# Kernel optimization log

Measured on AMD Instinct MI355X. Metric: run time of the kernel, lower is better.

Reference implementation:

```python
import jax, jax.numpy as jnp
import numpy as np

EPS = 1e-8
TAU = 0.2
IOU_THR = 0.5
NEG = -1e9
N, C, H, D_FG, D_CLS = 8192, 1024, 256, 64, 128


def setup_inputs() -> dict:
    key = jax.random.key(0)
    ks = jax.random.split(key, 11)
    def lin(k, fan_in, fan_out):
        return jax.random.normal(k, (fan_in, fan_out), jnp.float32) / np.sqrt(fan_in)
    return {
        "roi_feats": jax.random.normal(ks[0], (N, C), jnp.float32),
        "labels": jax.random.randint(ks[1], (N,), 0, 21, jnp.int32).astype(jnp.int64),
        "ious": jax.random.uniform(ks[2], (N,), jnp.float32),
        "fg_w1": lin(ks[3], C, H), "fg_b1": jnp.zeros((H,), jnp.float32),
        "fg_w2": lin(ks[4], H, D_FG), "fg_b2": jnp.zeros((D_FG,), jnp.float32),
        "cls_w1": lin(ks[5], C, H), "cls_b1": jnp.zeros((H,), jnp.float32),
        "cls_w2": lin(ks[6], H, D_CLS), "cls_b2": jnp.zeros((D_CLS,), jnp.float32),
    }


def _project_normalize(x, w1, b1, w2, b2):
    h = jax.nn.relu(x @ w1 + b1)
    z = h @ w2 + b2
    norm = jnp.maximum(jnp.linalg.norm(z, axis=1, keepdims=True), EPS)
    return z / norm


def _forward(roi_feats, labels, ious, fg_w1, fg_b1, fg_w2, fg_b2, cls_w1, cls_b1, cls_w2, cls_b2):
    n = roi_feats.shape[0]
    z_fg = _project_normalize(roi_feats, fg_w1, fg_b1, fg_w2, fg_b2)
    z_cls = _project_normalize(roi_feats, cls_w1, cls_b1, cls_w2, cls_b2)

    ignore = labels == -1
    fg = (labels > 0) & ~ignore
    iou_weight = jnp.where(ious > IOU_THR, ious, 0.0)
    eye = jnp.eye(n, dtype=bool)

    # ---- fg/bg contrastive (bg_as_negatives_only=True) ----
    sim_fg = (z_fg @ z_fg.T) / TAU                       # [N,N]
    exp_sim = jnp.exp(sim_fg)
    denom = jnp.sum(exp_sim * (~eye).astype(jnp.float32), axis=1)
    pos = (fg & ~ignore)[None, :] & ~eye                 # positives: fg columns, no self
    n_pos = jnp.sum(pos, axis=1)
    numer = jnp.sum(exp_sim * pos.astype(jnp.float32), axis=1)
    # original computes den = denom + EPS then -log((numer+EPS)/(den+EPS))
    loss_i = -jnp.log((numer + EPS) / (denom + 2.0 * EPS))
    valid = (fg & ~ignore) & (n_pos > 0)
    w = iou_weight * valid.astype(jnp.float32)
    loss_fg_bg = jnp.sum(w * loss_i) / (jnp.sum(w) + EPS)

    # ---- class supervised contrastive ----
    sim_cls = (z_cls @ z_cls.T) / TAU
    sim_masked = jnp.where(eye, NEG, sim_cls)
    log_denom = jax.nn.logsumexp(sim_masked, axis=1)     # [N]
    log_p = jnp.where(eye, NEG, sim_cls - log_denom[:, None])
    # pos_mask keeps diagonal (as in original): same label, col not ignore, col label != 0
    posc = (labels[None, :] == labels[:, None]) & (~ignore)[None, :] & (labels[None, :] != 0)
    n_posc = jnp.sum(posc, axis=1).astype(jnp.float32)
    sum_log_p = jnp.sum(log_p * posc.astype(jnp.float32), axis=1)
    valid_c = (fg & ~ignore) & (n_posc > 0) & jnp.isfinite(log_denom)
    Lzi = jnp.where(valid_c, -sum_log_p / (n_posc + EPS), 0.0)
    wc = iou_weight * valid_c.astype(jnp.float32)
    loss_supcon = jnp.sum(wc * Lzi) / (jnp.sum(wc) + EPS)

    return jnp.stack([loss_fg_bg, loss_supcon])


def reference(roi_feats, labels, ious, fg_w1, fg_b1, fg_w2, fg_b2, cls_w1, cls_b1, cls_w2, cls_b2):
    return _forward(roi_feats, labels, ious, fg_w1, fg_b1, fg_w2, fg_b2, cls_w1, cls_b1, cls_w2, cls_b2)
```

## Files before the change

### kernel.cpp

```cpp
#include <hip/hip_runtime.h>


typedef __attribute__((ext_vector_type(8))) short bs8;
typedef __attribute__((ext_vector_type(4))) float f4;

#define MFMA_BF16(a, b, c) __builtin_amdgcn_mfma_f32_16x16x32_bf16((a), (b), (c), 0, 0, 0)

#if defined(__has_builtin)
#if __has_builtin(__builtin_amdgcn_exp2f)
#define EXP2F(x) __builtin_amdgcn_exp2f(x)
#endif
#endif
#ifndef EXP2F
#define EXP2F(x) exp2f(x)
#endif

#define K_LOG2E 7.2134752044448170f

__device__ __forceinline__ unsigned short f2bf(float f) {
  unsigned int u = __float_as_uint(f);
  u = (u + 0x7fffu + ((u >> 16) & 1u)) >> 16;
  return (unsigned short)u;
}
__device__ __forceinline__ float bf2f(unsigned short s) {
  return __uint_as_float(((unsigned int)s) << 16);
}

constexpr size_t O_W1T  = 0;
constexpr size_t O_W2TF = 1048576;
constexpr size_t O_W2TC = 1081344;
constexpr size_t O_H    = 1146880;
constexpr size_t O_ZF   = 9535488;
constexpr size_t O_ZC   = 10584064;
constexpr size_t O_SCLS = 12681216;
constexpr size_t O_ROWD = 12697600;
constexpr size_t O_ROWN = 12730368;
constexpr size_t O_ROWS = 12763136;
constexpr size_t O_SCAL = 12795904;
constexpr size_t O_HIST = 12795920;
constexpr size_t O_NFG  = 12796048;
constexpr int ZERO_WORDS = (int)((O_NFG + 4 - O_SCLS) / 4);

__global__ void __launch_bounds__(256) zero_kernel(float* __restrict__ p, int n) {
  int i = blockIdx.x * 256 + threadIdx.x;
  if (i < n) p[i] = 0.f;
}

__global__ void __launch_bounds__(256) transp_kernel(
    const float* __restrict__ fgw1, const float* __restrict__ clsw1,
    const float* __restrict__ fgw2, const float* __restrict__ clsw2,
    unsigned short* __restrict__ W1T, unsigned short* __restrict__ W2Tf,
    unsigned short* __restrict__ W2Tc) {
  __shared__ float tile[64][65];
  const int m = blockIdx.y;
  const float* src;
  unsigned short* dst;
  int R, C;
  if (m == 0)      { src = fgw1;  dst = W1T;              R = 1024; C = 256; }
  else if (m == 1) { src = clsw1; dst = W1T + 256 * 1024; R = 1024; C = 256; }
  else if (m == 2) { src = fgw2;  dst = W2Tf;             R = 256;  C = 64;  }
  else             { src = clsw2; dst = W2Tc;             R = 256;  C = 128; }
  const int cT = C >> 6;
  if (blockIdx.x >= (R >> 6) * cT) return;
  const int r0 = (blockIdx.x / cT) << 6, c0 = (blockIdx.x % cT) << 6;
  const int t = threadIdx.x;
  {
    const int rr = t >> 4, cc = (t & 15) << 2;
#pragma unroll
    for (int i = 0; i < 4; i++) {
      float4 v = *(const float4*)(src + (size_t)(r0 + rr + i * 16) * C + c0 + cc);
      tile[rr + i * 16][cc] = v.x; tile[rr + i * 16][cc + 1] = v.y;
      tile[rr + i * 16][cc + 2] = v.z; tile[rr + i * 16][cc + 3] = v.w;
    }
  }
  __syncthreads();
  {
    const int dr = t >> 2, dc = (t & 3) << 4;
    bs8 o0, o1;
#pragma unroll
    for (int j = 0; j < 8; j++) o0[j] = (short)f2bf(tile[dc + j][dr]);
#pragma unroll
    for (int j = 0; j < 8; j++) o1[j] = (short)f2bf(tile[dc + 8 + j][dr]);
    unsigned short* dp = dst + (size_t)(c0 + dr) * R + r0 + dc;
    *(bs8*)dp = o0;
    *(bs8*)(dp + 8) = o1;
  }
}

__global__ void __launch_bounds__(256) meta_kernel(const int* __restrict__ labels,
                                                   int* __restrict__ hist,
                                                   int* __restrict__ nfg) {
  __shared__ int sh[33];
  const int t = threadIdx.x;
  if (t < 33) sh[t] = 0;
  __syncthreads();
  int lab = labels[blockIdx.x * 256 + t];
  if (lab >= 0 && lab < 32) atomicAdd(&sh[lab], 1);
  if (lab > 0) atomicAdd(&sh[32], 1);
  __syncthreads();
  if (t < 32 && sh[t] > 0) atomicAdd(&hist[t], sh[t]);
  if (t == 32 && sh[32] > 0) atomicAdd(nfg, sh[32]);
}

__global__ void __launch_bounds__(256) gemm1_kernel(
    const float* __restrict__ X, const unsigned short* __restrict__ W1T,
    const float* __restrict__ b1f, const float* __restrict__ b1c,
    unsigned short* __restrict__ H) {
  __shared__ __align__(16) unsigned short lA[64 * 40];
  __shared__ __align__(16) unsigned short lB[128 * 40];
  const int t = threadIdx.x;
  const int w = t >> 6, lane = t & 63, ln = lane & 15, quad = lane >> 4;
  const int m0 = blockIdx.x * 64, n0 = blockIdx.y * 128;

  f4 acc[8];
#pragma unroll
  for (int s = 0; s < 8; s++) acc[s] = (f4){0.f, 0.f, 0.f, 0.f};

  for (int k0 = 0; k0 < 1024; k0 += 32) {
    __syncthreads();
    {
      const int r = t >> 2, c = (t & 3) * 8;
      const float* xp = X + (size_t)(m0 + r) * 1024 + k0 + c;
      float4 x0 = *(const float4*)xp;
      float4 x1 = *(const float4*)(xp + 4);
      bs8 av;
      av[0] = (short)f2bf(x0.x); av[1] = (short)f2bf(x0.y);
      av[2] = (short)f2bf(x0.z); av[3] = (short)f2bf(x0.w);
      av[4] = (short)f2bf(x1.x); av[5] = (short)f2bf(x1.y);
      av[6] = (short)f2bf(x1.z); av[7] = (short)f2bf(x1.w);
      *(bs8*)&lA[r * 40 + c] = av;
    }
#pragma unroll
    for (int i = 0; i < 2; i++) {
      const int ch = t + i * 256;
      const int r = ch >> 2, c = (ch & 3) * 8;
      *(bs8*)&lB[r * 40 + c] = *(const bs8*)(W1T + (size_t)(n0 + r) * 1024 + k0 + c);
    }
    __syncthreads();
    bs8 af = *(const bs8*)&lA[(w * 16 + ln) * 40 + quad * 8];
#pragma unroll
    for (int s = 0; s < 8; s++) {
      bs8 bf = *(const bs8*)&lB[(s * 16 + ln) * 40 + quad * 8];
      acc[s] = MFMA_BF16(af, bf, acc[s]);
    }
  }
#pragma unroll
  for (int s = 0; s < 8; s++) {
    const int n = n0 + s * 16 + ln;
    const float b = (n < 256) ? b1f[n] : b1c[n - 256];
#pragma unroll
    for (int r = 0; r < 4; r++) {
      float v = fmaxf(acc[s][r] + b, 0.f);
      H[(size_t)(m0 + w * 16 + quad * 4 + r) * 512 + n] = f2bf(v);
    }
  }
}

__global__ void __launch_bounds__(256) gemm2_kernel(
    const unsigned short* __restrict__ H,
    const unsigned short* __restrict__ W2Tf, const unsigned short* __restrict__ W2Tc,
    const float* __restrict__ b2f, const float* __restrict__ b2c,
    unsigned short* __restrict__ Zf, unsigned short* __restrict__ Zc) {
  const int t = threadIdx.x;
  const int w = t >> 6, lane = t & 63, ln = lane & 15, quad = lane >> 4;
  const int rw = blockIdx.x * 32 + (w & 1) * 16;

  if (w < 2) {
    const unsigned short* hrow = H + (size_t)(rw + ln) * 512;
    f4 acc[4];
#pragma unroll
    for (int s = 0; s < 4; s++) acc[s] = (f4){0.f, 0.f, 0.f, 0.f};
#pragma unroll
    for (int ks = 0; ks < 8; ks++) {
      bs8 af = *(const bs8*)(hrow + ks * 32 + quad * 8);
#pragma unroll
      for (int s = 0; s < 4; s++) {
        bs8 bf = *(const bs8*)(W2Tf + (size_t)(s * 16 + ln) * 256 + ks * 32 + quad * 8);
        acc[s] = MFMA_BF16(af, bf, acc[s]);
      }
    }
    float ss[4] = {0.f, 0.f, 0.f, 0.f};
#pragma unroll
    for (int s = 0; s < 4; s++) {
      float b = b2f[s * 16 + ln];
#pragma unroll
      for (int r = 0; r < 4; r++) {
        acc[s][r] += b;
        ss[r] = fmaf(acc[s][r], acc[s][r], ss[r]);
      }
    }
#pragma unroll
    for (int r = 0; r < 4; r++) {
#pragma unroll
      for (int off = 1; off < 16; off <<= 1) ss[r] += __shfl_xor(ss[r], off, 64);
      float sc = 1.f / fmaxf(sqrtf(ss[r]), 1e-8f);
#pragma unroll
      for (int s = 0; s < 4; s++)
        Zf[(size_t)(rw + quad * 4 + r) * 64 + s * 16 + ln] = f2bf(acc[s][r] * sc);
    }
  } else {
    const unsigned short* hrow = H + (size_t)(rw + ln) * 512 + 256;
    f4 acc[8];
#pragma unroll
    for (int s = 0; s < 8; s++) acc[s] = (f4){0.f, 0.f, 0.f, 0.f};
#pragma unroll
    for (int ks = 0; ks < 8; ks++) {
      bs8 af = *(const bs8*)(hrow + ks * 32 + quad * 8);
#pragma unroll
      for (int s = 0; s < 8; s++) {
        bs8 bf = *(const bs8*)(W2Tc + (size_t)(s * 16 + ln) * 256 + ks * 32 + quad * 8);
        acc[s] = MFMA_BF16(af, bf, acc[s]);
      }
    }
    float ss[4] = {0.f, 0.f, 0.f, 0.f};
#pragma unroll
    for (int s = 0; s < 8; s++) {
      float b = b2c[s * 16 + ln];
#pragma unroll
      for (int r = 0; r < 4; r++) {
        acc[s][r] += b;
        ss[r] = fmaf(acc[s][r], acc[s][r], ss[r]);
      }
    }
#pragma unroll
    for (int r = 0; r < 4; r++) {
#pragma unroll
      for (int off = 1; off < 16; off <<= 1) ss[r] += __shfl_xor(ss[r], off, 64);
      float sc = 1.f / fmaxf(sqrtf(ss[r]), 1e-8f);
#pragma unroll
      for (int s = 0; s < 8; s++)
        Zc[(size_t)(rw + quad * 4 + r) * 128 + s * 16 + ln] = f2bf(acc[s][r] * sc);
    }
  }
}

__global__ void __launch_bounds__(128) scls_kernel(const unsigned short* __restrict__ Zc,
                                                   const int* __restrict__ labels,
                                                   float* __restrict__ Scls) {
  const int c = blockIdx.x + 1;
  const int t = threadIdx.x;
  const int r0 = blockIdx.y * 256;
  float acc = 0.f;
#pragma unroll 4
  for (int r = r0; r < r0 + 256; r++) {
    if (labels[r] == c) acc += bf2f(Zc[(size_t)r * 128 + t]);
  }
  atomicAdd(&Scls[c * 128 + t], acc);
}

__global__ void __launch_bounds__(256) sim_kernel(
    const unsigned short* __restrict__ Zf, const unsigned short* __restrict__ Zc,
    const int* __restrict__ labels,
    float* __restrict__ rowD, float* __restrict__ rowN, float* __restrict__ rowS) {
  const int bi = blockIdx.x, y = blockIdx.y;
  const int dlo = (y == 0) ? 0 : 2 * y - 1;
  const int dhi = (y == 0) ? 0 : 2 * y;

  __shared__ __align__(16) unsigned short sZf[64 * 72];
  __shared__ __align__(16) unsigned short sZc[64 * 136];
  __shared__ float sFg[64];
  __shared__ float sCol[4][2][4][16][3];
  const int t = threadIdx.x;
  const int w = t >> 6, lane = t & 63, ln = lane & 15, quad = lane >> 4;
  const int rbase = bi * 128 + w * 32;

  bs8 afg[2][2], acl[2][4];
  float fgr[2][4];
#pragma unroll
  for (int rs = 0; rs < 2; rs++) {
    const unsigned short* zf = Zf + (size_t)(rbase + rs * 16 + ln) * 64;
    const unsigned short* zc = Zc + (size_t)(rbase + rs * 16 + ln) * 128;
#pragma unroll
    for (int s = 0; s < 2; s++) afg[rs][s] = *(const bs8*)(zf + s * 32 + quad * 8);
#pragma unroll
    for (int s = 0; s < 4; s++) acl[rs][s] = *(const bs8*)(zc + s * 32 + quad * 8);
#pragma unroll
    for (int r = 0; r < 4; r++)
      fgr[rs][r] = (labels[rbase + rs * 16 + quad * 4 + r] > 0) ? 1.f : 0.f;
  }

  float dacc[2][4] = {}, nacc[2][4] = {}, sacc[2][4] = {};

  for (int d = dlo; d <= dhi; d++) {
    if (d == 32 && bi >= 32) break;
    const int bj = (bi + d) & 63;
    const bool diag = (d == 0);
    float cd[2][4] = {}, cn[2][4] = {}, cs[2][4] = {};

#pragma unroll
    for (int ct = 0; ct < 2; ct++) {
      const int c0 = bj * 128 + ct * 64;
      __syncthreads();
#pragma unroll
      for (int i = 0; i < 2; i++) {
        int ch = t + i * 256;
        int j = ch >> 3, c8 = (ch & 7) * 8;
        *(bs8*)&sZf[j * 72 + c8] = *(const bs8*)(Zf + (size_t)(c0 + j) * 64 + c8);
      }
#pragma unroll
      for (int i = 0; i < 4; i++) {
        int ch = t + i * 256;
        int j = ch >> 4, c8 = (ch & 15) * 8;
        *(bs8*)&sZc[j * 136 + c8] = *(const bs8*)(Zc + (size_t)(c0 + j) * 128 + c8);
      }
      if (t < 64) sFg[t] = (labels[c0 + t] > 0) ? 1.f : 0.f;
      __syncthreads();

#pragma unroll
      for (int s = 0; s < 4; s++) {
        const int lcol = s * 16 + ln;
        const float fgc = sFg[lcol];
        bs8 b0 = *(const bs8*)&sZf[lcol * 72 + quad * 8];
        bs8 b1 = *(const bs8*)&sZf[lcol * 72 + 32 + quad * 8];
#pragma unroll
        for (int rs = 0; rs < 2; rs++) {
          f4 c = {0.f, 0.f, 0.f, 0.f};
          c = MFMA_BF16(afg[rs][0], b0, c);
          c = MFMA_BF16(afg[rs][1], b1, c);
#pragma unroll
          for (int r = 0; r < 4; r++) {
            float e = EXP2F(c[r] * K_LOG2E);
            dacc[rs][r] += e;
            nacc[rs][r] = fmaf(fgc, e, nacc[rs][r]);
            cd[ct][s] += e;
            cn[ct][s] = fmaf(fgr[rs][r], e, cn[ct][s]);
          }
        }
        bs8 bc0 = *(const bs8*)&sZc[lcol * 136 + quad * 8];
        bs8 bc1 = *(const bs8*)&sZc[lcol * 136 + 32 + quad * 8];
        bs8 bc2 = *(const bs8*)&sZc[lcol * 136 + 64 + quad * 8];
        bs8 bc3 = *(const bs8*)&sZc[lcol * 136 + 96 + quad * 8];
#pragma unroll
        for (int rs = 0; rs < 2; rs++) {
          f4 c = {0.f, 0.f, 0.f, 0.f};
          c = MFMA_BF16(acl[rs][0], bc0, c);
          c = MFMA_BF16(acl[rs][1], bc1, c);
          c = MFMA_BF16(acl[rs][2], bc2, c);
          c = MFMA_BF16(acl[rs][3], bc3, c);
#pragma unroll
          for (int r = 0; r < 4; r++) {
            float e = EXP2F(c[r] * K_LOG2E);
            sacc[rs][r] += e;
            cs[ct][s] += e;
          }
        }
      }
    }

    if (!diag) {
#pragma unroll
      for (int ct = 0; ct < 2; ct++)
#pragma unroll
        for (int s = 0; s < 4; s++) {
          float dv = cd[ct][s], nv = cn[ct][s], sv = cs[ct][s];
#pragma unroll
          for (int off = 16; off < 64; off <<= 1) {
            dv += __shfl_xor(dv, off, 64);
            nv += __shfl_xor(nv, off, 64);
            sv += __shfl_xor(sv, off, 64);
          }
          if (quad == 0) {
            sCol[w][ct][s][ln][0] = dv;
            sCol[w][ct][s][ln][1] = nv;
            sCol[w][ct][s][ln][2] = sv;
          }
        }
      __syncthreads();
      if (t < 128) {
        const int ct = t >> 6, s = (t >> 4) & 3, lm = t & 15;
        float dv = 0.f, nv = 0.f, sv = 0.f;
#pragma unroll
        for (int ww = 0; ww < 4; ww++) {
          dv += sCol[ww][ct][s][lm][0];
          nv += sCol[ww][ct][s][lm][1];
          sv += sCol[ww][ct][s][lm][2];
        }
        const int col = bj * 128 + t;
        atomicAdd(&rowD[col], dv);
        atomicAdd(&rowN[col], nv);
        atomicAdd(&rowS[col], sv);
      }
    }
  }

#pragma unroll
  for (int rs = 0; rs < 2; rs++)
#pragma unroll
    for (int r = 0; r < 4; r++) {
      float dv = dacc[rs][r], nv = nacc[rs][r], sv = sacc[rs][r];
#pragma unroll
      for (int off = 1; off < 16; off <<= 1) {
        dv += __shfl_xor(dv, off, 64);
        nv += __shfl_xor(nv, off, 64);
        sv += __shfl_xor(sv, off, 64);
      }
      if (ln == 0) {
        int row = rbase + rs * 16 + quad * 4 + r;
        atomicAdd(&rowD[row], dv);
        atomicAdd(&rowN[row], nv);
        atomicAdd(&rowS[row], sv);
      }
    }
}

__global__ void __launch_bounds__(256) finalize_kernel(
    const unsigned short* __restrict__ Zf, const unsigned short* __restrict__ Zc,
    const int* __restrict__ labels, const float* __restrict__ ious,
    const float* __restrict__ rowD, const float* __restrict__ rowN,
    const float* __restrict__ rowS, const float* __restrict__ Scls,
    const int* __restrict__ hist, const int* __restrict__ nfg,
    float* __restrict__ scal) {
  __shared__ float red[4][4];
  const int t = threadIdx.x, w = t >> 6, lane = t & 63;
  float aw0 = 0.f, al0 = 0.f, aw1 = 0.f, al1 = 0.f;
  const int NFG = *nfg;
  for (int it = 0; it < 16; it++) {
    const int i = it * 512 + blockIdx.x * 4 + w;
    const int lab = labels[i];
    if (lab > 0 && lab < 32) {
      const float iou = ious[i];
      const float iw = (iou > 0.5f) ? iou : 0.f;
      float dot = 0.f, ssq = 0.f;
#pragma unroll
      for (int p = 0; p < 2; p++) {
        const int k = lane + p * 64;
        const float z = bf2f(Zc[(size_t)i * 128 + k]);
        dot = fmaf(z, Scls[lab * 128 + k], dot);
        ssq = fmaf(z, z, ssq);
      }
      float zf = bf2f(Zf[(size_t)i * 64 + lane]);
      float ssqf = zf * zf;
#pragma unroll
      for (int off = 1; off < 64; off <<= 1) {
        dot += __shfl_xor(dot, off, 64);
        ssq += __shfl_xor(ssq, off, 64);
        ssqf += __shfl_xor(ssqf, off, 64);
      }
      if (lane == 0) {
        const float ef = EXP2F(K_LOG2E * ssqf);
        if (NFG - 1 > 0) {
          const float D = rowD[i] - ef;
          const float Nn = rowN[i] - ef;
          const float loss = logf(D + 2e-8f) - logf(Nn + 1e-8f);
          aw0 += iw;
          al0 += iw * loss;
        }
        const int npc = hist[lab];
        if (npc > 0) {
          const float S = rowS[i] - EXP2F(K_LOG2E * ssq);
          const float logden = logf(S);
          const float slp = (dot - ssq) * 5.0f - (float)(npc - 1) * logden - 1e9f;
          aw1 += iw;
          al1 += iw * (-slp / ((float)npc + 1e-8f));
        }
      }
    }
  }
  if (lane == 0) { red[w][0] = aw0; red[w][1] = al0; red[w][2] = aw1; red[w][3] = al1; }
  __syncthreads();
  if (t < 4) atomicAdd(&scal[t], red[0][t] + red[1][t] + red[2][t] + red[3][t]);
}

__global__ void writeout_kernel(const float* __restrict__ scal, float* __restrict__ out) {
  if (threadIdx.x == 0) {
    out[0] = scal[1] / (scal[0] + 1e-8f);
    out[1] = scal[3] / (scal[2] + 1e-8f);
  }
}

extern "C" void kernel_launch(void* const* d_in, const int* in_sizes, int n_in,
                              void* d_out, int out_size, void* d_ws, size_t ws_size,
                              hipStream_t stream) {
  (void)in_sizes; (void)n_in; (void)out_size; (void)ws_size;
  const float* roi    = (const float*)d_in[0];
  const int*   labels = (const int*)d_in[1];
  const float* ious   = (const float*)d_in[2];
  const float* fgw1   = (const float*)d_in[3];
  const float* fgb1   = (const float*)d_in[4];
  const float* fgw2   = (const float*)d_in[5];
  const float* fgb2   = (const float*)d_in[6];
  const float* clsw1  = (const float*)d_in[7];
  const float* clsb1  = (const float*)d_in[8];
  const float* clsw2  = (const float*)d_in[9];
  const float* clsb2  = (const float*)d_in[10];

  char* ws = (char*)d_ws;
  unsigned short* W1T  = (unsigned short*)(ws + O_W1T);
  unsigned short* W2Tf = (unsigned short*)(ws + O_W2TF);
  unsigned short* W2Tc = (unsigned short*)(ws + O_W2TC);
  unsigned short* Hb   = (unsigned short*)(ws + O_H);
  unsigned short* Zf   = (unsigned short*)(ws + O_ZF);
  unsigned short* Zc   = (unsigned short*)(ws + O_ZC);
  float* Scls = (float*)(ws + O_SCLS);
  float* rowD = (float*)(ws + O_ROWD);
  float* rowN = (float*)(ws + O_ROWN);
  float* rowS = (float*)(ws + O_ROWS);
  float* scal = (float*)(ws + O_SCAL);
  int* hist = (int*)(ws + O_HIST);
  int* nfg  = (int*)(ws + O_NFG);
  float* out = (float*)d_out;

  hipLaunchKernelGGL(zero_kernel, dim3((ZERO_WORDS + 255) / 256), dim3(256), 0, stream,
                     (float*)(ws + O_SCLS), ZERO_WORDS);
  hipLaunchKernelGGL(transp_kernel, dim3(64, 4), dim3(256), 0, stream,
                     fgw1, clsw1, fgw2, clsw2, W1T, W2Tf, W2Tc);
  hipLaunchKernelGGL(meta_kernel, dim3(32), dim3(256), 0, stream, labels, hist, nfg);
  hipLaunchKernelGGL(gemm1_kernel, dim3(128, 4), dim3(256), 0, stream,
                     roi, W1T, fgb1, clsb1, Hb);
  hipLaunchKernelGGL(gemm2_kernel, dim3(256), dim3(256), 0, stream,
                     Hb, W2Tf, W2Tc, fgb2, clsb2, Zf, Zc);
  hipLaunchKernelGGL(scls_kernel, dim3(20, 32), dim3(128), 0, stream, Zc, labels, Scls);
  hipLaunchKernelGGL(sim_kernel, dim3(64, 17), dim3(256), 0, stream,
                     Zf, Zc, labels, rowD, rowN, rowS);
  hipLaunchKernelGGL(finalize_kernel, dim3(128), dim3(256), 0, stream,
                     Zf, Zc, labels, ious, rowD, rowN, rowS, Scls, hist, nfg, scal);
  hipLaunchKernelGGL(writeout_kernel, dim3(1), dim3(64), 0, stream, scal, out);
}
```

Measured before the change: 233.9 us.

## Split similarity kernel into fg and cls kernels and merge prep launches

```diff
diff --git a/kernel.cpp b/kernel.cpp
--- a/kernel.cpp
+++ b/kernel.cpp
@@ -39,20 +39,43 @@
 constexpr size_t O_SCAL = 12795904;
 constexpr size_t O_HIST = 12795920;
 constexpr size_t O_NFG  = 12796048;
-constexpr int ZERO_WORDS = (int)((O_NFG + 4 - O_SCLS) / 4);
-
-__global__ void __launch_bounds__(256) zero_kernel(float* __restrict__ p, int n) {
-  int i = blockIdx.x * 256 + threadIdx.x;
-  if (i < n) p[i] = 0.f;
-}
-
-__global__ void __launch_bounds__(256) transp_kernel(
+constexpr int ZERO_WORDS = (int)((O_SCAL + 16 - O_SCLS) / 4);
+
+__global__ void __launch_bounds__(256) prep_kernel(
     const float* __restrict__ fgw1, const float* __restrict__ clsw1,
     const float* __restrict__ fgw2, const float* __restrict__ clsw2,
+    const int* __restrict__ labels,
     unsigned short* __restrict__ W1T, unsigned short* __restrict__ W2Tf,
-    unsigned short* __restrict__ W2Tc) {
+    unsigned short* __restrict__ W2Tc,
+    int* __restrict__ hist, int* __restrict__ nfg, float* __restrict__ zp) {
+  const int b = blockIdx.x;
+  const int t = threadIdx.x;
+
+  if (b >= 141) {
+    const int i = (b - 141) * 256 + t;
+    if (i < ZERO_WORDS) zp[i] = 0.f;
+    return;
+  }
+  if (b == 140) {
+    __shared__ int sh[33];
+    if (t < 33) sh[t] = 0;
+    __syncthreads();
+    for (int it = 0; it < 32; it++) {
+      const int lab = labels[it * 256 + t];
+      if (lab >= 0 && lab < 32) atomicAdd(&sh[lab], 1);
+      if (lab > 0) atomicAdd(&sh[32], 1);
+    }
+    __syncthreads();
+    if (t < 32) hist[t] = sh[t];
+    if (t == 32) *nfg = sh[32];
+    return;
+  }
+  int m, tb;
+  if (b < 64)       { m = 0; tb = b; }
+  else if (b < 128) { m = 1; tb = b - 64; }
+  else if (b < 132) { m = 2; tb = b - 128; }
+  else              { m = 3; tb = b - 132; }
   __shared__ float tile[64][65];
-  const int m = blockIdx.y;
   const float* src;
   unsigned short* dst;
   int R, C;
@@ -61,9 +84,7 @@
   else if (m == 2) { src = fgw2;  dst = W2Tf;             R = 256;  C = 64;  }
   else             { src = clsw2; dst = W2Tc;             R = 256;  C = 128; }
   const int cT = C >> 6;
-  if (blockIdx.x >= (R >> 6) * cT) return;
-  const int r0 = (blockIdx.x / cT) << 6, c0 = (blockIdx.x % cT) << 6;
-  const int t = threadIdx.x;
+  const int r0 = (tb / cT) << 6, c0 = (tb % cT) << 6;
   {
     const int rr = t >> 4, cc = (t & 15) << 2;
 #pragma unroll
@@ -85,21 +106,6 @@
     *(bs8*)dp = o0;
     *(bs8*)(dp + 8) = o1;
   }
-}
-
-__global__ void __launch_bounds__(256) meta_kernel(const int* __restrict__ labels,
-                                                   int* __restrict__ hist,
-                                                   int* __restrict__ nfg) {
-  __shared__ int sh[33];
-  const int t = threadIdx.x;
-  if (t < 33) sh[t] = 0;
-  __syncthreads();
-  int lab = labels[blockIdx.x * 256 + t];
-  if (lab >= 0 && lab < 32) atomicAdd(&sh[lab], 1);
-  if (lab > 0) atomicAdd(&sh[32], 1);
-  __syncthreads();
-  if (t < 32 && sh[t] > 0) atomicAdd(&hist[t], sh[t]);
-  if (t == 32 && sh[32] > 0) atomicAdd(nfg, sh[32]);
 }
 
 __global__ void __launch_bounds__(256) gemm1_kernel(
@@ -248,138 +254,100 @@
   atomicAdd(&Scls[c * 128 + t], acc);
 }
 
-__global__ void __launch_bounds__(256) sim_kernel(
-    const unsigned short* __restrict__ Zf, const unsigned short* __restrict__ Zc,
-    const int* __restrict__ labels,
-    float* __restrict__ rowD, float* __restrict__ rowN, float* __restrict__ rowS) {
-  const int bi = blockIdx.x, y = blockIdx.y;
-  const int dlo = (y == 0) ? 0 : 2 * y - 1;
-  const int dhi = (y == 0) ? 0 : 2 * y;
+__global__ void __launch_bounds__(256) simfg_kernel(
+    const unsigned short* __restrict__ Zf, const int* __restrict__ labels,
+    float* __restrict__ rowD, float* __restrict__ rowN) {
+  const int bi = blockIdx.x, d = blockIdx.y;
+  if (d == 32 && bi >= 32) return;
+  const int bj = (bi + d) & 63;
+  const bool diag = (d == 0);
 
   __shared__ __align__(16) unsigned short sZf[64 * 72];
-  __shared__ __align__(16) unsigned short sZc[64 * 136];
   __shared__ float sFg[64];
-  __shared__ float sCol[4][2][4][16][3];
+  __shared__ float sCol[4][2][4][16][2];
   const int t = threadIdx.x;
   const int w = t >> 6, lane = t & 63, ln = lane & 15, quad = lane >> 4;
   const int rbase = bi * 128 + w * 32;
 
-  bs8 afg[2][2], acl[2][4];
+  bs8 afg[2][2];
   float fgr[2][4];
 #pragma unroll
   for (int rs = 0; rs < 2; rs++) {
     const unsigned short* zf = Zf + (size_t)(rbase + rs * 16 + ln) * 64;
-    const unsigned short* zc = Zc + (size_t)(rbase + rs * 16 + ln) * 128;
 #pragma unroll
     for (int s = 0; s < 2; s++) afg[rs][s] = *(const bs8*)(zf + s * 32 + quad * 8);
-#pragma unroll
-    for (int s = 0; s < 4; s++) acl[rs][s] = *(const bs8*)(zc + s * 32 + quad * 8);
 #pragma unroll
     for (int r = 0; r < 4; r++)
       fgr[rs][r] = (labels[rbase + rs * 16 + quad * 4 + r] > 0) ? 1.f : 0.f;
   }
 
-  float dacc[2][4] = {}, nacc[2][4] = {}, sacc[2][4] = {};
-
-  for (int d = dlo; d <= dhi; d++) {
-    if (d == 32 && bi >= 32) break;
-    const int bj = (bi + d) & 63;
-    const bool diag = (d == 0);
-    float cd[2][4] = {}, cn[2][4] = {}, cs[2][4] = {};
-
-#pragma unroll
-    for (int ct = 0; ct < 2; ct++) {
-      const int c0 = bj * 128 + ct * 64;
-      __syncthreads();
-#pragma unroll
-      for (int i = 0; i < 2; i++) {
-        int ch = t + i * 256;
-        int j = ch >> 3, c8 = (ch & 7) * 8;
-        *(bs8*)&sZf[j * 72 + c8] = *(const bs8*)(Zf + (size_t)(c0 + j) * 64 + c8);
-      }
-#pragma unroll
-      for (int i = 0; i < 4; i++) {
-        int ch = t + i * 256;
-        int j = ch >> 4, c8 = (ch & 15) * 8;
-        *(bs8*)&sZc[j * 136 + c8] = *(const bs8*)(Zc + (size_t)(c0 + j) * 128 + c8);
-      }
-      if (t < 64) sFg[t] = (labels[c0 + t] > 0) ? 1.f : 0.f;
-      __syncthreads();
-
+  float dacc[2][4] = {}, nacc[2][4] = {};
+  float cd[2][4] = {}, cn[2][4] = {};
+
+#pragma unroll
+  for (int ct = 0; ct < 2; ct++) {
+    const int c0 = bj * 128 + ct * 64;
+    __syncthreads();
+#pragma unroll
+    for (int i = 0; i < 2; i++) {
+      int ch = t + i * 256;
+      int j = ch >> 3, c8 = (ch & 7) * 8;
+      *(bs8*)&sZf[j * 72 + c8] = *(const bs8*)(Zf + (size_t)(c0 + j) * 64 + c8);
+    }
+    if (t < 64) sFg[t] = (labels[c0 + t] > 0) ? 1.f : 0.f;
+    __syncthreads();
+
+#pragma unroll
+    for (int s = 0; s < 4; s++) {
+      const int lcol = s * 16 + ln;
+      const float fgc = sFg[lcol];
+      bs8 b0 = *(const bs8*)&sZf[lcol * 72 + quad * 8];
+      bs8 b1 = *(const bs8*)&sZf[lcol * 72 + 32 + quad * 8];
+#pragma unroll
+      for (int rs = 0; rs < 2; rs++) {
+        f4 c = {0.f, 0.f, 0.f, 0.f};
+        c = MFMA_BF16(afg[rs][0], b0, c);
+        c = MFMA_BF16(afg[rs][1], b1, c);
+#pragma unroll
+        for (int r = 0; r < 4; r++) {
+          float e = EXP2F(c[r] * K_LOG2E);
+          dacc[rs][r] += e;
+          nacc[rs][r] = fmaf(fgc, e, nacc[rs][r]);
+          cd[ct][s] += e;
+          cn[ct][s] = fmaf(fgr[rs][r], e, cn[ct][s]);
+        }
+      }
+    }
+  }
+
+  if (!diag) {
+#pragma unroll
+    for (int ct = 0; ct < 2; ct++)
 #pragma unroll
       for (int s = 0; s < 4; s++) {
-        const int lcol = s * 16 + ln;
-        const float fgc = sFg[lcol];
-        bs8 b0 = *(const bs8*)&sZf[lcol * 72 + quad * 8];
-        bs8 b1 = *(const bs8*)&sZf[lcol * 72 + 32 + quad * 8];
-#pragma unroll
-        for (int rs = 0; rs < 2; rs++) {
-          f4 c = {0.f, 0.f, 0.f, 0.f};
-          c = MFMA_BF16(afg[rs][0], b0, c);
-          c = MFMA_BF16(afg[rs][1], b1, c);
-#pragma unroll
-          for (int r = 0; r < 4; r++) {
-            float e = EXP2F(c[r] * K_LOG2E);
-            dacc[rs][r] += e;
-            nacc[rs][r] = fmaf(fgc, e, nacc[rs][r]);
-            cd[ct][s] += e;
-            cn[ct][s] = fmaf(fgr[rs][r], e, cn[ct][s]);
-          }
+        float dv = cd[ct][s], nv = cn[ct][s];
+#pragma unroll
+        for (int off = 16; off < 64; off <<= 1) {
+          dv += __shfl_xor(dv, off, 64);
+          nv += __shfl_xor(nv, off, 64);
         }
-        bs8 bc0 = *(const bs8*)&sZc[lcol * 136 + quad * 8];
-        bs8 bc1 = *(const bs8*)&sZc[lcol * 136 + 32 + quad * 8];
-        bs8 bc2 = *(const bs8*)&sZc[lcol * 136 + 64 + quad * 8];
-        bs8 bc3 = *(const bs8*)&sZc[lcol * 136 + 96 + quad * 8];
-#pragma unroll
-        for (int rs = 0; rs < 2; rs++) {
-          f4 c = {0.f, 0.f, 0.f, 0.f};
-          c = MFMA_BF16(acl[rs][0], bc0, c);
-          c = MFMA_BF16(acl[rs][1], bc1, c);
-          c = MFMA_BF16(acl[rs][2], bc2, c);
-          c = MFMA_BF16(acl[rs][3], bc3, c);
-#pragma unroll
-          for (int r = 0; r < 4; r++) {
-            float e = EXP2F(c[r] * K_LOG2E);
-            sacc[rs][r] += e;
-            cs[ct][s] += e;
-          }
+        if (quad == 0) {
+          sCol[w][ct][s][ln][0] = dv;
+          sCol[w][ct][s][ln][1] = nv;
         }
       }
-    }
-
-    if (!diag) {
-#pragma unroll
-      for (int ct = 0; ct < 2; ct++)
-#pragma unroll
-        for (int s = 0; s < 4; s++) {
-          float dv = cd[ct][s], nv = cn[ct][s], sv = cs[ct][s];
-#pragma unroll
-          for (int off = 16; off < 64; off <<= 1) {
-            dv += __shfl_xor(dv, off, 64);
-            nv += __shfl_xor(nv, off, 64);
-            sv += __shfl_xor(sv, off, 64);
-          }
-          if (quad == 0) {
-            sCol[w][ct][s][ln][0] = dv;
-            sCol[w][ct][s][ln][1] = nv;
-            sCol[w][ct][s][ln][2] = sv;
-          }
-        }
-      __syncthreads();
-      if (t < 128) {
-        const int ct = t >> 6, s = (t >> 4) & 3, lm = t & 15;
-        float dv = 0.f, nv = 0.f, sv = 0.f;
-#pragma unroll
-        for (int ww = 0; ww < 4; ww++) {
-          dv += sCol[ww][ct][s][lm][0];
-          nv += sCol[ww][ct][s][lm][1];
-          sv += sCol[ww][ct][s][lm][2];
-        }
-        const int col = bj * 128 + t;
-        atomicAdd(&rowD[col], dv);
-        atomicAdd(&rowN[col], nv);
-        atomicAdd(&rowS[col], sv);
-      }
+    __syncthreads();
+    if (t < 128) {
+      const int ct = t >> 6, s = (t >> 4) & 3, lm = t & 15;
+      float dv = 0.f, nv = 0.f;
+#pragma unroll
+      for (int ww = 0; ww < 4; ww++) {
+        dv += sCol[ww][ct][s][lm][0];
+        nv += sCol[ww][ct][s][lm][1];
+      }
+      const int col = bj * 128 + t;
+      atomicAdd(&rowD[col], dv);
+      atomicAdd(&rowN[col], nv);
     }
   }
 
@@ -387,19 +355,109 @@
   for (int rs = 0; rs < 2; rs++)
 #pragma unroll
     for (int r = 0; r < 4; r++) {
-      float dv = dacc[rs][r], nv = nacc[rs][r], sv = sacc[rs][r];
+      float dv = dacc[rs][r], nv = nacc[rs][r];
 #pragma unroll
       for (int off = 1; off < 16; off <<= 1) {
         dv += __shfl_xor(dv, off, 64);
         nv += __shfl_xor(nv, off, 64);
-        sv += __shfl_xor(sv, off, 64);
       }
       if (ln == 0) {
         int row = rbase + rs * 16 + quad * 4 + r;
         atomicAdd(&rowD[row], dv);
         atomicAdd(&rowN[row], nv);
-        atomicAdd(&rowS[row], sv);
-      }
+      }
+    }
+}
+
+__global__ void __launch_bounds__(256) simcls_kernel(
+    const unsigned short* __restrict__ Zc, float* __restrict__ rowS) {
+  const int bi = blockIdx.x, d = blockIdx.y;
+  if (d == 32 && bi >= 32) return;
+  const int bj = (bi + d) & 63;
+  const bool diag = (d == 0);
+
+  __shared__ __align__(16) unsigned short sZc[64 * 136];
+  __shared__ float sCol[4][2][4][16];
+  const int t = threadIdx.x;
+  const int w = t >> 6, lane = t & 63, ln = lane & 15, quad = lane >> 4;
+  const int rbase = bi * 128 + w * 32;
+
+  bs8 acl[2][4];
+#pragma unroll
+  for (int rs = 0; rs < 2; rs++) {
+    const unsigned short* zc = Zc + (size_t)(rbase + rs * 16 + ln) * 128;
+#pragma unroll
+    for (int s = 0; s < 4; s++) acl[rs][s] = *(const bs8*)(zc + s * 32 + quad * 8);
+  }
+
+  float sacc[2][4] = {};
+  float cs[2][4] = {};
+
+#pragma unroll
+  for (int ct = 0; ct < 2; ct++) {
+    const int c0 = bj * 128 + ct * 64;
+    __syncthreads();
+#pragma unroll
+    for (int i = 0; i < 4; i++) {
+      int ch = t + i * 256;
+      int j = ch >> 4, c8 = (ch & 15) * 8;
+      *(bs8*)&sZc[j * 136 + c8] = *(const bs8*)(Zc + (size_t)(c0 + j) * 128 + c8);
+    }
+    __syncthreads();
+
+#pragma unroll
+    for (int s = 0; s < 4; s++) {
+      const int lcol = s * 16 + ln;
+      bs8 bc0 = *(const bs8*)&sZc[lcol * 136 + quad * 8];
+      bs8 bc1 = *(const bs8*)&sZc[lcol * 136 + 32 + quad * 8];
+      bs8 bc2 = *(const bs8*)&sZc[lcol * 136 + 64 + quad * 8];
+      bs8 bc3 = *(const bs8*)&sZc[lcol * 136 + 96 + quad * 8];
+#pragma unroll
+      for (int rs = 0; rs < 2; rs++) {
+        f4 c = {0.f, 0.f, 0.f, 0.f};
+        c = MFMA_BF16(acl[rs][0], bc0, c);
+        c = MFMA_BF16(acl[rs][1], bc1, c);
+        c = MFMA_BF16(acl[rs][2], bc2, c);
+        c = MFMA_BF16(acl[rs][3], bc3, c);
+#pragma unroll
+        for (int r = 0; r < 4; r++) {
+          float e = EXP2F(c[r] * K_LOG2E);
+          sacc[rs][r] += e;
+          cs[ct][s] += e;
+        }
+      }
+    }
+  }
+
+  if (!diag) {
+#pragma unroll
+    for (int ct = 0; ct < 2; ct++)
+#pragma unroll
+      for (int s = 0; s < 4; s++) {
+        float sv = cs[ct][s];
+#pragma unroll
+        for (int off = 16; off < 64; off <<= 1) sv += __shfl_xor(sv, off, 64);
+        if (quad == 0) sCol[w][ct][s][ln] = sv;
+      }
+    __syncthreads();
+    if (t < 128) {
+      const int ct = t >> 6, s = (t >> 4) & 3, lm = t & 15;
+      float sv = 0.f;
+#pragma unroll
+      for (int ww = 0; ww < 4; ww++) sv += sCol[ww][ct][s][lm];
+      atomicAdd(&rowS[bj * 128 + t], sv);
+    }
+  }
+
+#pragma unroll
+  for (int rs = 0; rs < 2; rs++)
+#pragma unroll
+    for (int r = 0; r < 4; r++) {
+      float sv = sacc[rs][r];
+#pragma unroll
+      for (int off = 1; off < 16; off <<= 1) sv += __shfl_xor(sv, off, 64);
+      if (ln == 0)
+        atomicAdd(&rowS[rbase + rs * 16 + quad * 4 + r], sv);
     }
 }
 
@@ -500,18 +558,17 @@
   int* nfg  = (int*)(ws + O_NFG);
   float* out = (float*)d_out;
 
-  hipLaunchKernelGGL(zero_kernel, dim3((ZERO_WORDS + 255) / 256), dim3(256), 0, stream,
-                     (float*)(ws + O_SCLS), ZERO_WORDS);
-  hipLaunchKernelGGL(transp_kernel, dim3(64, 4), dim3(256), 0, stream,
-                     fgw1, clsw1, fgw2, clsw2, W1T, W2Tf, W2Tc);
-  hipLaunchKernelGGL(meta_kernel, dim3(32), dim3(256), 0, stream, labels, hist, nfg);
+  hipLaunchKernelGGL(prep_kernel, dim3(254), dim3(256), 0, stream,
+                     fgw1, clsw1, fgw2, clsw2, labels, W1T, W2Tf, W2Tc,
+                     hist, nfg, (float*)(ws + O_SCLS));
   hipLaunchKernelGGL(gemm1_kernel, dim3(128, 4), dim3(256), 0, stream,
                      roi, W1T, fgb1, clsb1, Hb);
   hipLaunchKernelGGL(gemm2_kernel, dim3(256), dim3(256), 0, stream,
                      Hb, W2Tf, W2Tc, fgb2, clsb2, Zf, Zc);
   hipLaunchKernelGGL(scls_kernel, dim3(20, 32), dim3(128), 0, stream, Zc, labels, Scls);
-  hipLaunchKernelGGL(sim_kernel, dim3(64, 17), dim3(256), 0, stream,
-                     Zf, Zc, labels, rowD, rowN, rowS);
+  hipLaunchKernelGGL(simfg_kernel, dim3(64, 33), dim3(256), 0, stream,
+                     Zf, labels, rowD, rowN);
+  hipLaunchKernelGGL(simcls_kernel, dim3(64, 33), dim3(256), 0, stream, Zc, rowS);
   hipLaunchKernelGGL(finalize_kernel, dim3(128), dim3(256), 0, stream,
                      Zf, Zc, labels, ious, rowD, rowN, rowS, Scls, hist, nfg, scal);
   hipLaunchKernelGGL(writeout_kernel, dim3(1), dim3(64), 0, stream, scal, out);
```

After: 220.3 us. 5.8% less time.
